# Kernel optimization log

Hardware: AMD Instinct MI355X
Metric: run time of the kernel (lower is better)

## Reference

```python
import jax, jax.numpy as jnp
import numpy as np

N_EMB = 1024
N_HEADS = 16
HS = N_EMB // N_HEADS  # 64
BASE = 10000.0


def _rope_cache(T):
    # theta uses dim = n_emb (as in the source), sliced to hs//2 frequencies
    i = jnp.arange(HS // 2, dtype=jnp.float32)
    theta = BASE ** (-2.0 * i / N_EMB)            # [hs/2]
    pos = jnp.arange(T, dtype=jnp.float32)        # [T]
    ang = pos[:, None] * theta[None, :]           # [T, hs/2]
    return jnp.cos(ang), jnp.sin(ang)


def _apply_rope(x, cos, sin):
    # x: [B, T, nh, hs]; rotate consecutive pairs along hs
    b, t, nh, hs = x.shape
    xr = x.reshape(b, t, nh, hs // 2, 2)
    c = cos[None, :, None, :]
    s = sin[None, :, None, :]
    r0 = xr[..., 0] * c - xr[..., 1] * s
    r1 = xr[..., 1] * c + xr[..., 0] * s
    return jnp.stack([r0, r1], axis=-1).reshape(b, t, nh, hs)


def setup_inputs() -> dict:
    key = jax.random.key(0)
    k1, k2, k3, k4 = jax.random.split(key, 4)
    B, T = 2, 2048
    w_std = 0.02
    x = jax.random.normal(k1, (B, T, N_EMB), jnp.float32)
    Wq = jax.random.normal(k2, (N_EMB, N_EMB), jnp.float32) * w_std
    Wk = jax.random.normal(k3, (N_EMB, N_EMB), jnp.float32) * w_std
    Wv = jax.random.normal(k4, (N_EMB, N_EMB), jnp.float32) * w_std
    return {"x": x, "Wq": Wq, "Wk": Wk, "Wv": Wv}


def reference(x, Wq, Wk, Wv):
    B, T, C = x.shape
    # nn.Linear(bias=False): y = x @ W.T
    q = (x @ Wq.T).reshape(B, T, N_HEADS, HS)
    k = (x @ Wk.T).reshape(B, T, N_HEADS, HS)
    v = (x @ Wv.T).reshape(B, T, N_HEADS, HS)
    cos, sin = _rope_cache(T)
    q = _apply_rope(q, cos, sin)
    k = _apply_rope(k, cos, sin)
    # scale uses C (n_emb), as in the source (not head_size)
    wei = jnp.einsum('bqhd,bkhd->bhqk', q, k) * (C ** -0.5)  # [B, nh, T, T]
    mask = jnp.tril(jnp.ones((T, T), dtype=bool))
    wei = jnp.where(mask[None, None], wei, -jnp.inf)
    wei = jax.nn.softmax(wei, axis=-1)
    # dropout is identity in eval mode
    out = jnp.einsum('bhqk,bkhd->bqhd', wei, v).reshape(B, T, C)
    return out
```

## Files before the change

### kernel.cpp

```cpp
#include <hip/hip_runtime.h>
#include <stdint.h>

typedef unsigned short u16;
typedef __bf16 bf16x8 __attribute__((ext_vector_type(8)));
typedef unsigned short u16x8 __attribute__((ext_vector_type(8)));
typedef unsigned short u16x4 __attribute__((ext_vector_type(4)));
typedef float f32x4 __attribute__((ext_vector_type(4)));
typedef uint32_t u32v4 __attribute__((ext_vector_type(4)));

#define LOG2E 1.4426950408889634f

typedef const __attribute__((address_space(1))) uint32_t as1_u32;
typedef __attribute__((address_space(3))) uint32_t as3_u32;

__device__ __forceinline__ u16 f2bf(float f) {
  union { float f; uint32_t i; } v; v.f = f;
  uint32_t r = (v.i + 0x7fffu + ((v.i >> 16) & 1u)) >> 16;
  return (u16)r;
}
__device__ __forceinline__ float bf2f(u16 u) {
  union { uint32_t i; float f; } v; v.i = ((uint32_t)u) << 16; return v.f;
}

__device__ __forceinline__ void gld_lds16(const void* g, void* l) {
  as1_u32* gp = (as1_u32*)((uintptr_t)g);
  as3_u32* lp = (as3_u32*)(uint32_t)(uintptr_t)(l);
  __builtin_amdgcn_global_load_lds(gp, lp, 16, 0, 0);
}

__global__ __launch_bounds__(256) void f32_to_bf16(
    const float* __restrict__ x, const float* __restrict__ wq,
    const float* __restrict__ wk, const float* __restrict__ wv,
    u16* __restrict__ xc, u16* __restrict__ wqc,
    u16* __restrict__ wkc, u16* __restrict__ wvc) {
  const int z = blockIdx.y;
  const float* src = z == 0 ? x : (z == 1 ? wq : (z == 2 ? wk : wv));
  u16* dst = z == 0 ? xc : (z == 1 ? wqc : (z == 2 ? wkc : wvc));
  const int n = z == 0 ? (1 << 22) : (1 << 20);

  const int idx = (blockIdx.x * 256 + (int)threadIdx.x) * 8;
  if (idx >= n) return;
  const f32x4 a = *(const f32x4*)&src[idx];
  const f32x4 b = *(const f32x4*)&src[idx + 4];
  u16x8 o;
#pragma unroll
  for (int j = 0; j < 4; j++) { o[j] = f2bf(a[j]); o[j + 4] = f2bf(b[j]); }
  *(u16x8*)&dst[idx] = o;
}

__global__ __launch_bounds__(256) void qkv_gemm(
    const u16* __restrict__ xc, const u16* __restrict__ wqc,
    const u16* __restrict__ wkc, const u16* __restrict__ wvc,
    u16* __restrict__ qo, u16* __restrict__ ko, u16* __restrict__ vt) {
  __shared__ __align__(16) u16 As[128 * 32];
  __shared__ __align__(16) u16 Bs[128 * 32];

  const int tid = threadIdx.x;
  const int lane = tid & 63;
  const int w = tid >> 6;
  const int wm = w >> 1, wn = w & 1;
  const int quad = lane >> 4, m16 = lane & 15;
  const int which = blockIdx.z;

  const u16* __restrict__ Ap;
  const u16* __restrict__ Bp;
  int m0, n0;
  if (which == 2) {
    Ap = wvc; Bp = xc;
    m0 = blockIdx.x * 128;
    n0 = blockIdx.y * 128;
  } else {
    Ap = xc; Bp = which == 0 ? wqc : wkc;
    m0 = blockIdx.y * 128;
    n0 = blockIdx.x * 128;
  }

  const f32x4 z4 = {0.f, 0.f, 0.f, 0.f};
  f32x4 acc[4][4];
#pragma unroll
  for (int i = 0; i < 4; i++)
#pragma unroll
    for (int j = 0; j < 4; j++) acc[i][j] = z4;

  const int rowA = m0 + w * 32 + (lane >> 2);
  const int rowB = n0 + w * 32 + (lane >> 2);
  const int cch = (lane & 3) * 8;

  for (int k0 = 0; k0 < 1024; k0 += 32) {
    __syncthreads();
#pragma unroll
    for (int i = 0; i < 2; i++) {
      gld_lds16(&Ap[(size_t)(rowA + i * 16) * 1024 + k0 + cch],
                &As[(w * 32 + i * 16) * 32]);
      gld_lds16(&Bp[(size_t)(rowB + i * 16) * 1024 + k0 + cch],
                &Bs[(w * 32 + i * 16) * 32]);
    }
    __syncthreads();

    bf16x8 af[4], bfr[4];
#pragma unroll
    for (int t = 0; t < 4; t++) {
      af[t]  = *(const bf16x8*)&As[(wm * 64 + t * 16 + m16) * 32 + quad * 8];
      bfr[t] = *(const bf16x8*)&Bs[(wn * 64 + t * 16 + m16) * 32 + quad * 8];
    }
#pragma unroll
    for (int mt = 0; mt < 4; mt++)
#pragma unroll
      for (int nt = 0; nt < 4; nt++)
        acc[mt][nt] = __builtin_amdgcn_mfma_f32_16x16x32_bf16(
            af[mt], bfr[nt], acc[mt][nt], 0, 0, 0);
  }

  if (which < 2) {
    u16* __restrict__ out = which == 0 ? qo : ko;
#pragma unroll
    for (int mt = 0; mt < 4; mt++) {
      const int row = m0 + wm * 64 + mt * 16 + quad * 4;
#pragma unroll
      for (int nt = 0; nt < 4; nt++) {
        const int n = n0 + wn * 64 + nt * 16 + m16;
        f32x4 a = acc[mt][nt];
#pragma unroll
        for (int r = 0; r < 4; r++)
          out[(size_t)(row + r) * 1024 + n] = f2bf(a[r]);
      }
    }
  } else {
#pragma unroll
    for (int mt = 0; mt < 4; mt++) {
      const int row = m0 + wm * 64 + mt * 16 + quad * 4;
#pragma unroll
      for (int nt = 0; nt < 4; nt++) {
        const int n = n0 + wn * 64 + nt * 16 + m16;
        f32x4 a = acc[mt][nt];
#pragma unroll
        for (int r = 0; r < 4; r++)
          vt[(size_t)(row + r) * 4096 + n] = f2bf(a[r]);
      }
    }
  }
}

__global__ __launch_bounds__(256) void rope_inplace(u16* __restrict__ qb,
                                                    u16* __restrict__ kb) {
  u16* buf = blockIdx.y == 0 ? qb : kb;
  const int p = blockIdx.x * 256 + (int)threadIdx.x;
  const int nidx = p * 2;
  const int row = nidx >> 10;
  const int col = nidx & 1023;
  const int i = (col & 63) >> 1;
  const int t = row & 2047;
  const float theta = exp2f(-(float)i * 0.02595256324130752f);
  const float ang = (float)t * theta;
  float s, c;
  sincosf(ang, &s, &c);
  const float a0 = bf2f(buf[(size_t)row * 1024 + col]);
  const float a1 = bf2f(buf[(size_t)row * 1024 + col + 1]);
  buf[(size_t)row * 1024 + col]     = f2bf(a0 * c - a1 * s);
  buf[(size_t)row * 1024 + col + 1] = f2bf(a1 * c + a0 * s);
}

__global__ __launch_bounds__(256) void flash_attn(
    const u16* __restrict__ qg, const u16* __restrict__ kg,
    const u16* __restrict__ vt, float* __restrict__ out) {
  __shared__ __align__(16) u16 Qs[64 * 72];
  __shared__ __align__(16) u16 Ks[64 * 72];
  __shared__ __align__(16) u16 Vs[64 * 72];

  const int tid = threadIdx.x, lane = tid & 63, w = tid >> 6;
  const int quad = lane >> 4, m16 = lane & 15;
  const int h = blockIdx.y, b = blockIdx.z;
  const size_t base = (size_t)b * 2048 * 1024 + (size_t)h * 64;
  const size_t vbase = (size_t)(h * 64) * 4096 + (size_t)b * 2048;
  const float SC = 0.03125f * LOG2E;

  const f32x4 z4 = {0.f, 0.f, 0.f, 0.f};
  const int srow = tid >> 2, sc = (tid & 3) * 16;

  for (int pass = 0; pass < 2; ++pass) {
    const int qt = pass == 0 ? (int)blockIdx.x : 31 - (int)blockIdx.x;
    const int q0 = qt * 64;

    __syncthreads();
    {
      const u16* src = &qg[base + (size_t)(q0 + srow) * 1024 + sc];
      *(u16x8*)&Qs[srow * 72 + sc] = *(const u16x8*)src;
      *(u16x8*)&Qs[srow * 72 + sc + 8] = *(const u16x8*)(src + 8);
    }
    u16x8 kr0, kr1, vr0, vr1;
    {
      const u16* ks = &kg[base + (size_t)srow * 1024 + sc];
      kr0 = *(const u16x8*)ks; kr1 = *(const u16x8*)(ks + 8);
      const u16* vs = &vt[vbase + (size_t)srow * 4096 + sc];
      vr0 = *(const u16x8*)vs; vr1 = *(const u16x8*)(vs + 8);
    }
    __syncthreads();
    const bf16x8 qf0 = *(const bf16x8*)&Qs[(w * 16 + m16) * 72 + quad * 8];
    const bf16x8 qf1 = *(const bf16x8*)&Qs[(w * 16 + m16) * 72 + 32 + quad * 8];

    float l_p = 0.f;
    f32x4 O[4];
#pragma unroll
    for (int d = 0; d < 4; d++) O[d] = z4;

    const int qrow0 = q0 + w * 16 + quad * 4;
    const int qcol  = q0 + w * 16 + m16;

    for (int kt = 0; kt <= qt; ++kt) {
      const int k0 = kt * 64;
      if (kt) __syncthreads();
      *(u16x8*)&Ks[srow * 72 + sc] = kr0;
      *(u16x8*)&Ks[srow * 72 + sc + 8] = kr1;
      {
        const u16x4* v0 = (const u16x4*)&vr0;
        const u16x4* v1 = (const u16x4*)&vr1;
        *(u16x4*)&Vs[srow * 72 + sc]      = v0[0];
        *(u16x4*)&Vs[srow * 72 + sc + 4]  = v1[0];
        *(u16x4*)&Vs[srow * 72 + sc + 8]  = v0[1];
        *(u16x4*)&Vs[srow * 72 + sc + 12] = v1[1];
      }
      __syncthreads();
      if (kt < qt) {
        const u16* ks = &kg[base + (size_t)(k0 + 64 + srow) * 1024 + sc];
        kr0 = *(const u16x8*)ks; kr1 = *(const u16x8*)(ks + 8);
        const u16* vs = &vt[vbase + (size_t)srow * 4096 + k0 + 64 + sc];
        vr0 = *(const u16x8*)vs; vr1 = *(const u16x8*)(vs + 8);
      }

      f32x4 S[4];
#pragma unroll
      for (int nt = 0; nt < 4; nt++) {
        const bf16x8 kf0 = *(const bf16x8*)&Ks[(nt * 16 + m16) * 72 + quad * 8];
        const bf16x8 kf1 =
            *(const bf16x8*)&Ks[(nt * 16 + m16) * 72 + 32 + quad * 8];
        S[nt] = __builtin_amdgcn_mfma_f32_16x16x32_bf16(kf0, qf0, z4, 0, 0, 0);
        S[nt] = __builtin_amdgcn_mfma_f32_16x16x32_bf16(kf1, qf1, S[nt], 0, 0, 0);
      }

      const bool diag = (kt == qt);
      uint32_t W[8];
#pragma unroll
      for (int nt = 0; nt < 4; nt++) {
        float p[4];
#pragma unroll
        for (int r = 0; r < 4; r++) {
          float e = exp2f(S[nt][r] * SC);
          const int key = k0 + nt * 16 + quad * 4 + r;
          if (diag && key > qcol) e = 0.f;
          p[r] = e;
        }
        uint32_t w0, w1;
        asm("v_cvt_pk_bf16_f32 %0, %1, %2" : "=v"(w0) : "v"(p[0]), "v"(p[1]));
        asm("v_cvt_pk_bf16_f32 %0, %1, %2" : "=v"(w1) : "v"(p[2]), "v"(p[3]));
        W[2 * nt] = w0; W[2 * nt + 1] = w1;
        union { uint32_t i; float f; } e0, e1, e2, e3;
        e0.i = w0 << 16; e1.i = w0 & 0xffff0000u;
        e2.i = w1 << 16; e3.i = w1 & 0xffff0000u;
        l_p += (e0.f + e1.f) + (e2.f + e3.f);
      }

      uint32_t a0 = W[0], b0 = W[2], a1 = W[1], b1 = W[3];
      asm("v_permlane32_swap_b32 %0, %1" : "+v"(a0), "+v"(b0));
      asm("v_permlane32_swap_b32 %0, %1" : "+v"(a1), "+v"(b1));
      uint32_t a2 = W[4], b2 = W[6], a3 = W[5], b3 = W[7];
      asm("v_permlane32_swap_b32 %0, %1" : "+v"(a2), "+v"(b2));
      asm("v_permlane32_swap_b32 %0, %1" : "+v"(a3), "+v"(b3));
      union { u32v4 u; bf16x8 f; } P0, P1;
      P0.u = (u32v4){a0, a1, b0, b1};
      P1.u = (u32v4){a2, a3, b2, b3};

#pragma unroll
      for (int dt = 0; dt < 4; dt++) {
        const bf16x8 vf0 = *(const bf16x8*)&Vs[(dt * 16 + m16) * 72 + quad * 8];
        const bf16x8 vf1 =
            *(const bf16x8*)&Vs[(dt * 16 + m16) * 72 + 32 + quad * 8];
        O[dt] = __builtin_amdgcn_mfma_f32_16x16x32_bf16(P0.f, vf0, O[dt], 0, 0, 0);
        O[dt] = __builtin_amdgcn_mfma_f32_16x16x32_bf16(P1.f, vf1, O[dt], 0, 0, 0);
      }
    }

    l_p += __shfl_xor(l_p, 16);
    l_p += __shfl_xor(l_p, 32);
    float inv[4];
#pragma unroll
    for (int r = 0; r < 4; r++) inv[r] = 1.0f / __shfl(l_p, quad * 4 + r);

#pragma unroll
    for (int dt = 0; dt < 4; dt++)
#pragma unroll
      for (int r = 0; r < 4; r++)
        out[base + (size_t)(qrow0 + r) * 1024 + dt * 16 + m16] =
            O[dt][r] * inv[r];
  }
}

extern "C" void kernel_launch(void* const* d_in, const int* in_sizes, int n_in,
                              void* d_out, int out_size, void* d_ws, size_t ws_size,
                              hipStream_t stream) {
  const float* x  = (const float*)d_in[0];
  const float* Wq = (const float*)d_in[1];
  const float* Wk = (const float*)d_in[2];
  const float* Wv = (const float*)d_in[3];
  u16* qb  = (u16*)d_ws;
  u16* kb  = qb  + (size_t)4096 * 1024;
  u16* vtw = kb  + (size_t)4096 * 1024;
  u16* xc  = vtw + (size_t)4096 * 1024;
  u16* wqc = xc  + (size_t)4096 * 1024;
  u16* wkc = wqc + (size_t)1024 * 1024;
  u16* wvc = wkc + (size_t)1024 * 1024;

  f32_to_bf16<<<dim3(2048, 4), 256, 0, stream>>>(x, Wq, Wk, Wv,
                                                 xc, wqc, wkc, wvc);
  qkv_gemm<<<dim3(8, 32, 3), 256, 0, stream>>>(xc, wqc, wkc, wvc,
                                               qb, kb, vtw);
  rope_inplace<<<dim3(8192, 2), 256, 0, stream>>>(qb, kb);
  flash_attn<<<dim3(16, 16, 2), 256, 0, stream>>>(qb, kb, vtw, (float*)d_out);
}
```

Measured before the change: 167.7 us.

## Widen attention key tiles to 128, use MFMA row-sums, and swizzle blocks across XCDs

The flash attention loop now handles 128 keys per iteration instead of 64, with twice as many K/V registers prefetched. This halves the number of barrier-separated iterations, and the last iteration masks keys past the diagonal. The softmax denominator is now computed with an MFMA against a vector of bf16 ones, replacing the per-lane VALU sums and cross-lane shuffles. Blocks are launched as a flat 1D grid and remapped so that consecutive block ids spread across XCDs while tiles of the same head stay grouped, aiming at better L2 reuse. In exchange, LDS and register use go up and the masked tail work on even diagonals is wasted.

```diff
diff --git a/kernel.cpp b/kernel.cpp
--- a/kernel.cpp
+++ b/kernel.cpp
@@ -164,12 +164,18 @@
     const u16* __restrict__ qg, const u16* __restrict__ kg,
     const u16* __restrict__ vt, float* __restrict__ out) {
   __shared__ __align__(16) u16 Qs[64 * 72];
-  __shared__ __align__(16) u16 Ks[64 * 72];
-  __shared__ __align__(16) u16 Vs[64 * 72];
+  __shared__ __align__(16) u16 Ks[128 * 72];
+  __shared__ __align__(16) u16 Vs[64 * 136];
 
   const int tid = threadIdx.x, lane = tid & 63, w = tid >> 6;
   const int quad = lane >> 4, m16 = lane & 15;
-  const int h = blockIdx.y, b = blockIdx.z;
+
+  const int id  = (int)blockIdx.x;
+  const int wid = (id & 7) * 64 + (id >> 3);
+  const int xq  = wid & 15;
+  const int h   = (wid >> 4) & 15;
+  const int b   = wid >> 8;
+
   const size_t base = (size_t)b * 2048 * 1024 + (size_t)h * 64;
   const size_t vbase = (size_t)(h * 64) * 4096 + (size_t)b * 2048;
   const float SC = 0.03125f * LOG2E;
@@ -177,9 +183,14 @@
   const f32x4 z4 = {0.f, 0.f, 0.f, 0.f};
   const int srow = tid >> 2, sc = (tid & 3) * 16;
 
+  union { u16x8 u; bf16x8 f; } ones;
+#pragma unroll
+  for (int j = 0; j < 8; j++) ones.u[j] = 0x3F80;
+
   for (int pass = 0; pass < 2; ++pass) {
-    const int qt = pass == 0 ? (int)blockIdx.x : 31 - (int)blockIdx.x;
+    const int qt = pass == 0 ? xq : 31 - xq;
     const int q0 = qt * 64;
+    const int nr = (qt + 2) >> 1;
 
     __syncthreads();
     {
@@ -187,18 +198,21 @@
       *(u16x8*)&Qs[srow * 72 + sc] = *(const u16x8*)src;
       *(u16x8*)&Qs[srow * 72 + sc + 8] = *(const u16x8*)(src + 8);
     }
-    u16x8 kr0, kr1, vr0, vr1;
+    u16x8 kr0, kr1, kr2, kr3, vr0, vr1, vr2, vr3;
     {
       const u16* ks = &kg[base + (size_t)srow * 1024 + sc];
       kr0 = *(const u16x8*)ks; kr1 = *(const u16x8*)(ks + 8);
+      const u16* ks2 = ks + (size_t)64 * 1024;
+      kr2 = *(const u16x8*)ks2; kr3 = *(const u16x8*)(ks2 + 8);
       const u16* vs = &vt[vbase + (size_t)srow * 4096 + sc];
       vr0 = *(const u16x8*)vs; vr1 = *(const u16x8*)(vs + 8);
+      vr2 = *(const u16x8*)(vs + 64); vr3 = *(const u16x8*)(vs + 72);
     }
     __syncthreads();
     const bf16x8 qf0 = *(const bf16x8*)&Qs[(w * 16 + m16) * 72 + quad * 8];
     const bf16x8 qf1 = *(const bf16x8*)&Qs[(w * 16 + m16) * 72 + 32 + quad * 8];
 
-    float l_p = 0.f;
+    f32x4 l4 = z4;
     f32x4 O[4];
 #pragma unroll
     for (int d = 0; d < 4; d++) O[d] = z4;
@@ -206,30 +220,41 @@
     const int qrow0 = q0 + w * 16 + quad * 4;
     const int qcol  = q0 + w * 16 + m16;
 
-    for (int kt = 0; kt <= qt; ++kt) {
-      const int k0 = kt * 64;
-      if (kt) __syncthreads();
+    for (int rr = 0; rr < nr; ++rr) {
+      const int k0 = rr * 128;
+      if (rr) __syncthreads();
       *(u16x8*)&Ks[srow * 72 + sc] = kr0;
       *(u16x8*)&Ks[srow * 72 + sc + 8] = kr1;
+      *(u16x8*)&Ks[(64 + srow) * 72 + sc] = kr2;
+      *(u16x8*)&Ks[(64 + srow) * 72 + sc + 8] = kr3;
       {
         const u16x4* v0 = (const u16x4*)&vr0;
         const u16x4* v1 = (const u16x4*)&vr1;
-        *(u16x4*)&Vs[srow * 72 + sc]      = v0[0];
-        *(u16x4*)&Vs[srow * 72 + sc + 4]  = v1[0];
-        *(u16x4*)&Vs[srow * 72 + sc + 8]  = v0[1];
-        *(u16x4*)&Vs[srow * 72 + sc + 12] = v1[1];
+        *(u16x4*)&Vs[srow * 136 + sc]      = v0[0];
+        *(u16x4*)&Vs[srow * 136 + sc + 4]  = v1[0];
+        *(u16x4*)&Vs[srow * 136 + sc + 8]  = v0[1];
+        *(u16x4*)&Vs[srow * 136 + sc + 12] = v1[1];
+        const u16x4* v2 = (const u16x4*)&vr2;
+        const u16x4* v3 = (const u16x4*)&vr3;
+        *(u16x4*)&Vs[srow * 136 + 64 + sc]      = v2[0];
+        *(u16x4*)&Vs[srow * 136 + 64 + sc + 4]  = v3[0];
+        *(u16x4*)&Vs[srow * 136 + 64 + sc + 8]  = v2[1];
+        *(u16x4*)&Vs[srow * 136 + 64 + sc + 12] = v3[1];
       }
       __syncthreads();
-      if (kt < qt) {
-        const u16* ks = &kg[base + (size_t)(k0 + 64 + srow) * 1024 + sc];
+      if (rr + 1 < nr) {
+        const u16* ks = &kg[base + (size_t)(k0 + 128 + srow) * 1024 + sc];
         kr0 = *(const u16x8*)ks; kr1 = *(const u16x8*)(ks + 8);
-        const u16* vs = &vt[vbase + (size_t)srow * 4096 + k0 + 64 + sc];
+        const u16* ks2 = ks + (size_t)64 * 1024;
+        kr2 = *(const u16x8*)ks2; kr3 = *(const u16x8*)(ks2 + 8);
+        const u16* vs = &vt[vbase + (size_t)srow * 4096 + k0 + 128 + sc];
         vr0 = *(const u16x8*)vs; vr1 = *(const u16x8*)(vs + 8);
-      }
-
-      f32x4 S[4];
-#pragma unroll
-      for (int nt = 0; nt < 4; nt++) {
+        vr2 = *(const u16x8*)(vs + 64); vr3 = *(const u16x8*)(vs + 72);
+      }
+
+      f32x4 S[8];
+#pragma unroll
+      for (int nt = 0; nt < 8; nt++) {
         const bf16x8 kf0 = *(const bf16x8*)&Ks[(nt * 16 + m16) * 72 + quad * 8];
         const bf16x8 kf1 =
             *(const bf16x8*)&Ks[(nt * 16 + m16) * 72 + 32 + quad * 8];
@@ -237,53 +262,54 @@
         S[nt] = __builtin_amdgcn_mfma_f32_16x16x32_bf16(kf1, qf1, S[nt], 0, 0, 0);
       }
 
-      const bool diag = (kt == qt);
-      uint32_t W[8];
-#pragma unroll
-      for (int nt = 0; nt < 4; nt++) {
+      const bool lastr = (rr == nr - 1);
+      uint32_t W[16];
+#pragma unroll
+      for (int nt = 0; nt < 8; nt++) {
         float p[4];
 #pragma unroll
         for (int r = 0; r < 4; r++) {
           float e = exp2f(S[nt][r] * SC);
           const int key = k0 + nt * 16 + quad * 4 + r;
-          if (diag && key > qcol) e = 0.f;
+          if (lastr && key > qcol) e = 0.f;
           p[r] = e;
         }
         uint32_t w0, w1;
         asm("v_cvt_pk_bf16_f32 %0, %1, %2" : "=v"(w0) : "v"(p[0]), "v"(p[1]));
         asm("v_cvt_pk_bf16_f32 %0, %1, %2" : "=v"(w1) : "v"(p[2]), "v"(p[3]));
         W[2 * nt] = w0; W[2 * nt + 1] = w1;
-        union { uint32_t i; float f; } e0, e1, e2, e3;
-        e0.i = w0 << 16; e1.i = w0 & 0xffff0000u;
-        e2.i = w1 << 16; e3.i = w1 & 0xffff0000u;
-        l_p += (e0.f + e1.f) + (e2.f + e3.f);
-      }
-
-      uint32_t a0 = W[0], b0 = W[2], a1 = W[1], b1 = W[3];
-      asm("v_permlane32_swap_b32 %0, %1" : "+v"(a0), "+v"(b0));
-      asm("v_permlane32_swap_b32 %0, %1" : "+v"(a1), "+v"(b1));
-      uint32_t a2 = W[4], b2 = W[6], a3 = W[5], b3 = W[7];
-      asm("v_permlane32_swap_b32 %0, %1" : "+v"(a2), "+v"(b2));
-      asm("v_permlane32_swap_b32 %0, %1" : "+v"(a3), "+v"(b3));
-      union { u32v4 u; bf16x8 f; } P0, P1;
-      P0.u = (u32v4){a0, a1, b0, b1};
-      P1.u = (u32v4){a2, a3, b2, b3};
+      }
+
+      union { u32v4 u; bf16x8 f; } P[4];
+#pragma unroll
+      for (int ks = 0; ks < 4; ks++) {
+        uint32_t a0 = W[4 * ks], b0 = W[4 * ks + 2];
+        uint32_t a1 = W[4 * ks + 1], b1 = W[4 * ks + 3];
+        asm("v_permlane32_swap_b32 %0, %1" : "+v"(a0), "+v"(b0));
+        asm("v_permlane32_swap_b32 %0, %1" : "+v"(a1), "+v"(b1));
+        P[ks].u = (u32v4){a0, a1, b0, b1};
+      }
+
+#pragma unroll
+      for (int ks = 0; ks < 4; ks++)
+        l4 = __builtin_amdgcn_mfma_f32_16x16x32_bf16(P[ks].f, ones.f, l4,
+                                                     0, 0, 0);
 
 #pragma unroll
       for (int dt = 0; dt < 4; dt++) {
-        const bf16x8 vf0 = *(const bf16x8*)&Vs[(dt * 16 + m16) * 72 + quad * 8];
-        const bf16x8 vf1 =
-            *(const bf16x8*)&Vs[(dt * 16 + m16) * 72 + 32 + quad * 8];
-        O[dt] = __builtin_amdgcn_mfma_f32_16x16x32_bf16(P0.f, vf0, O[dt], 0, 0, 0);
-        O[dt] = __builtin_amdgcn_mfma_f32_16x16x32_bf16(P1.f, vf1, O[dt], 0, 0, 0);
-      }
-    }
-
-    l_p += __shfl_xor(l_p, 16);
-    l_p += __shfl_xor(l_p, 32);
+#pragma unroll
+        for (int ks = 0; ks < 4; ks++) {
+          const bf16x8 vf =
+              *(const bf16x8*)&Vs[(dt * 16 + m16) * 136 + ks * 32 + quad * 8];
+          O[dt] = __builtin_amdgcn_mfma_f32_16x16x32_bf16(P[ks].f, vf, O[dt],
+                                                          0, 0, 0);
+        }
+      }
+    }
+
     float inv[4];
 #pragma unroll
-    for (int r = 0; r < 4; r++) inv[r] = 1.0f / __shfl(l_p, quad * 4 + r);
+    for (int r = 0; r < 4; r++) inv[r] = 1.0f / l4[r];
 
 #pragma unroll
     for (int dt = 0; dt < 4; dt++)
@@ -314,5 +340,5 @@
   qkv_gemm<<<dim3(8, 32, 3), 256, 0, stream>>>(xc, wqc, wkc, wvc,
                                                qb, kb, vtw);
   rope_inplace<<<dim3(8192, 2), 256, 0, stream>>>(qb, kb);
-  flash_attn<<<dim3(16, 16, 2), 256, 0, stream>>>(qb, kb, vtw, (float*)d_out);
-}
+  flash_attn<<<dim3(512, 1, 1), 256, 0, stream>>>(qb, kb, vtw, (float*)d_out);
+}
```

After: 166.8 us. About the same (-0.6%).
